# Optimization experiments

Hardware: AMD Instinct MI355X
Metric: run time of the kernel (lower is better)

The kernel has to match this reference:

```python
import jax, jax.numpy as jnp
import numpy as np

EMBED_DIM = 512
NUM_HEADS = 8
HEAD_DIM = EMBED_DIM // NUM_HEADS
SCALING = HEAD_DIM ** (-0.5)
LAMBDA = 1.0
T = 128
B = 8


def setup_inputs() -> dict:
    key = jax.random.key(0)
    ks = jax.random.split(key, 8)
    d = EMBED_DIM
    # xavier-uniform-ish scale for weights
    w_lim = float(np.sqrt(6.0 / (3 * d + d)))
    o_lim = float(np.sqrt(6.0 / (d + d)))
    return {
        "query": jax.random.normal(ks[0], (T, B, d), jnp.float32),
        "key": jax.random.normal(ks[1], (T, B, d), jnp.float32),
        "value": jax.random.normal(ks[2], (T, B, d), jnp.float32),
        "correlation_bias": jax.random.normal(ks[3], (B, T, T, T), jnp.float32) * 0.1,
        "in_proj_weight": jax.random.uniform(ks[4], (3 * d, d), jnp.float32, -w_lim, w_lim),
        "in_proj_bias": jnp.zeros((3 * d,), jnp.float32),
        "out_w": jax.random.uniform(ks[5], (d, d), jnp.float32, -o_lim, o_lim),
        "out_b": jnp.zeros((d,), jnp.float32),
    }


def reference(query, key, value, correlation_bias, in_proj_weight, in_proj_bias, out_w, out_b):
    tgt_len, bsz, d = query.shape
    h, hd = NUM_HEADS, HEAD_DIM
    # split packed in-projection
    q = query @ in_proj_weight[:d].T + in_proj_bias[:d]
    k = key @ in_proj_weight[d:2 * d].T + in_proj_bias[d:2 * d]
    v = value @ in_proj_weight[2 * d:].T + in_proj_bias[2 * d:]
    q = q * SCALING
    # [T, B, D] -> [B*H, T, hd]
    q = q.reshape(tgt_len, bsz * h, hd).transpose(1, 0, 2)
    k = k.reshape(tgt_len, bsz * h, hd).transpose(1, 0, 2)
    v = v.reshape(tgt_len, bsz * h, hd).transpose(1, 0, 2)
    # trilinear score cube: [B*H, Tq, Tk, Tv]
    scores = jnp.einsum('iat,ibt,ict->iabc', q, k, v)
    # expand correlation bias over heads: [B,Tq,Tk,Tv] -> [B*H,Tq,Tk,Tv]
    bias = jnp.broadcast_to(
        correlation_bias[:, None], (bsz, h, tgt_len, tgt_len, tgt_len)
    ).reshape(bsz * h, tgt_len, tgt_len, tgt_len)
    scores = scores + LAMBDA * bias
    # mean/max fusion over Tv, softmax over Tk
    fused = jnp.mean(scores, axis=-1) + jnp.max(scores, axis=-1)
    w = jax.nn.softmax(fused.astype(jnp.float32), axis=-1).astype(fused.dtype)
    # bmm with q (note: attends over q itself, Tk == Tq required)
    attn = jnp.einsum('iab,ibd->iad', w, q)
    attn = attn.transpose(1, 0, 2).reshape(tgt_len, bsz, d)
    return attn @ out_w.T + out_b
```

## Files before the change

### kernel.cpp

```cpp
#include <hip/hip_runtime.h>
#include <math.h>

#define SCALING 0.125f

typedef __attribute__((ext_vector_type(8))) short short8;
typedef __attribute__((ext_vector_type(4))) float f32x4;

static __device__ __forceinline__ unsigned short bf16r(float x) {
  unsigned int u = __float_as_uint(x);
  u += 0x7fffu + ((u >> 16) & 1u);
  return (unsigned short)(u >> 16);
}
static __device__ __forceinline__ float bf16f(unsigned short h) {
  return __uint_as_float(((unsigned int)h) << 16);
}
static __device__ __forceinline__ unsigned int pk_bf16(float lo, float hi) {
  unsigned int ua = __float_as_uint(lo);
  unsigned int ub = __float_as_uint(hi);
  ua += 0x7fffu + ((ua >> 16) & 1u);
  ub += 0x7fffu + ((ub >> 16) & 1u);
  return __builtin_amdgcn_perm(ub, ua, 0x07060302u);
}
static __device__ __forceinline__ void split4(float4 x, ushort4& h, ushort4& l) {
  h.x = bf16r(x.x); l.x = bf16r(x.x - bf16f(h.x));
  h.y = bf16r(x.y); l.y = bf16r(x.y - bf16f(h.y));
  h.z = bf16r(x.z); l.z = bf16r(x.z - bf16f(h.z));
  h.w = bf16r(x.w); l.w = bf16r(x.w - bf16f(h.w));
}
union U4S8 { uint4 u; short8 s; };

__global__ __launch_bounds__(256)
void prep_kernel(const float* __restrict__ query,
                 const float* __restrict__ key,
                 const float* __restrict__ value,
                 const float* __restrict__ W,
                 const float* __restrict__ out_w,
                 unsigned short* __restrict__ Xh,
                 unsigned short* __restrict__ Xl,
                 unsigned short* __restrict__ Wh,
                 unsigned short* __restrict__ Wl,
                 unsigned short* __restrict__ Owh,
                 unsigned short* __restrict__ Owl) {
  const int t = blockIdx.x * 256 + threadIdx.x;
  const int e = t * 4;
  const float* __restrict__ src;
  unsigned short *dh, *dl;
  if (e < 1572864) {
    const int g = e >> 19, j = e & 524287;
    src = (g == 0 ? query : g == 1 ? key : value) + j;
    dh = Xh + e; dl = Xl + e;
  } else if (e < 2359296) {
    const int j = e - 1572864;
    src = W + j; dh = Wh + j; dl = Wl + j;
  } else {
    const int j = e - 2359296;
    src = out_w + j; dh = Owh + j; dl = Owl + j;
  }
  const float4 v = *(const float4*)src;
  ushort4 hh, ll;
  split4(v, hh, ll);
  *(ushort4*)dh = hh;
  *(ushort4*)dl = ll;
}

__global__ __launch_bounds__(256)
void projmm_kernel(const unsigned short* __restrict__ Xh,
                   const unsigned short* __restrict__ Xl,
                   const unsigned short* __restrict__ Wh,
                   const unsigned short* __restrict__ Wl,
                   const float* __restrict__ bias,
                   float* __restrict__ qh, float* __restrict__ kh,
                   unsigned short* __restrict__ vh) {
  __shared__ __align__(16) unsigned short Ah[64 * 72];
  __shared__ __align__(16) unsigned short Al[64 * 72];
  __shared__ __align__(16) unsigned short Bh[32 * 72];
  __shared__ __align__(16) unsigned short Bl[32 * 72];
  const int n0 = blockIdx.x * 32;
  const int g = n0 >> 9;
  const unsigned short* __restrict__ Xgh = Xh + g * 524288;
  const unsigned short* __restrict__ Xgl = Xl + g * 524288;
  const int m0 = blockIdx.y * 64;
  const int tid = threadIdx.x;
  const int w = tid >> 6, lane = tid & 63;
  const int quad = lane >> 4, n15 = lane & 15;
  const int srow = tid >> 2;
  const int scol = (tid & 3) * 16;
  const bool doB = tid >= 128;
  const int brow = (tid & 127) >> 2;
  const int bcol = (tid & 3) * 16;

  f32x4 acc[2];
#pragma unroll
  for (int nt = 0; nt < 2; ++nt) acc[nt] = (f32x4){0.f, 0.f, 0.f, 0.f};

  uint4 rah0, rah1, ral0, ral1, rbh0, rbh1, rbl0, rbl1;
  {
    const int ar = (m0 + srow) * 512 + scol;
    rah0 = *(const uint4*)&Xgh[ar];   rah1 = *(const uint4*)&Xgh[ar + 8];
    ral0 = *(const uint4*)&Xgl[ar];   ral1 = *(const uint4*)&Xgl[ar + 8];
  }
  if (doB) {
    const int br = (n0 + brow) * 512 + bcol;
    rbh0 = *(const uint4*)&Wh[br];    rbh1 = *(const uint4*)&Wh[br + 8];
    rbl0 = *(const uint4*)&Wl[br];    rbl1 = *(const uint4*)&Wl[br + 8];
  }

  for (int k0 = 0; k0 < 512; k0 += 64) {
    __syncthreads();
    *(uint4*)&Ah[srow * 72 + scol] = rah0; *(uint4*)&Ah[srow * 72 + scol + 8] = rah1;
    *(uint4*)&Al[srow * 72 + scol] = ral0; *(uint4*)&Al[srow * 72 + scol + 8] = ral1;
    if (doB) {
      *(uint4*)&Bh[brow * 72 + bcol] = rbh0; *(uint4*)&Bh[brow * 72 + bcol + 8] = rbh1;
      *(uint4*)&Bl[brow * 72 + bcol] = rbl0; *(uint4*)&Bl[brow * 72 + bcol + 8] = rbl1;
    }
    __syncthreads();
    if (k0 + 64 < 512) {
      const int ar = (m0 + srow) * 512 + k0 + 64 + scol;
      rah0 = *(const uint4*)&Xgh[ar]; rah1 = *(const uint4*)&Xgh[ar + 8];
      ral0 = *(const uint4*)&Xgl[ar]; ral1 = *(const uint4*)&Xgl[ar + 8];
      if (doB) {
        const int br = (n0 + brow) * 512 + k0 + 64 + bcol;
        rbh0 = *(const uint4*)&Wh[br]; rbh1 = *(const uint4*)&Wh[br + 8];
        rbl0 = *(const uint4*)&Wl[br]; rbl1 = *(const uint4*)&Wl[br + 8];
      }
    }
#pragma unroll
    for (int kk = 0; kk < 2; ++kk) {
      short8 ah = *(const short8*)&Ah[(w * 16 + n15) * 72 + kk * 32 + quad * 8];
      short8 al = *(const short8*)&Al[(w * 16 + n15) * 72 + kk * 32 + quad * 8];
#pragma unroll
      for (int nt = 0; nt < 2; ++nt) {
        short8 bh = *(const short8*)&Bh[(nt * 16 + n15) * 72 + kk * 32 + quad * 8];
        short8 bl = *(const short8*)&Bl[(nt * 16 + n15) * 72 + kk * 32 + quad * 8];
        acc[nt] = __builtin_amdgcn_mfma_f32_16x16x32_bf16(ah, bh, acc[nt], 0, 0, 0);
        acc[nt] = __builtin_amdgcn_mfma_f32_16x16x32_bf16(ah, bl, acc[nt], 0, 0, 0);
        acc[nt] = __builtin_amdgcn_mfma_f32_16x16x32_bf16(al, bh, acc[nt], 0, 0, 0);
      }
    }
  }

#pragma unroll
  for (int nt = 0; nt < 2; ++nt) {
    const int j = n0 + nt * 16 + n15;
    const int jj = j & 511;
    const int head = jj >> 6;
    const int hd = jj & 63;
    const float bj = bias[j];
#pragma unroll
    for (int r = 0; r < 4; ++r) {
      const int row = m0 + w * 16 + quad * 4 + r;
      const int t = row >> 3;
      const int batch = row & 7;
      const int i = batch * 8 + head;
      const int idx = ((i << 7) + t) * 64 + hd;
      const float val = acc[nt][r] + bj;
      if (g == 0)      qh[idx] = val * SCALING;
      else if (g == 1) kh[idx] = val;
      else             vh[idx] = bf16r(val);
    }
  }
}

__global__ __launch_bounds__(256, 2)
void score_kernel(const float* __restrict__ qh,
                  const float* __restrict__ kh,
                  const unsigned short* __restrict__ vh,
                  const float* __restrict__ cbias,
                  unsigned short* __restrict__ attn_h,
                  unsigned short* __restrict__ attn_l) {
  __shared__ __align__(16) unsigned short Ks[2][128 * 72];
  __shared__ __align__(16) unsigned short Vs[2][128 * 72];
  __shared__ float rowS[8 * 128];

  const int ab = blockIdx.x;
  const int batch = ab >> 7;
  const int a = ab & 127;
  const int tid = threadIdx.x;
  const int w = tid >> 6;
  const int lane = tid & 63;
  const int quad = lane >> 4;
  const int n15 = lane & 15;
  const int col8 = (tid & 7) * 8;

  const float* __restrict__ bp = cbias + (size_t)ab * 16384;
  f32x4 biasReg[8][2];
#pragma unroll
  for (int ic = 0; ic < 8; ++ic)
#pragma unroll
    for (int jb = 0; jb < 2; ++jb) {
      const int b = w * 32 + jb * 16 + n15;
      biasReg[ic][jb] = *(const f32x4*)&bp[b * 128 + ic * 16 + quad * 4];
    }

  {
    const int i = batch * 8;
    const float* __restrict__ kb = kh + (size_t)i * 8192;
    const uint4* __restrict__ vb4 = (const uint4*)(vh + (size_t)i * 8192);
    const float* __restrict__ qa = qh + ((size_t)i * 128 + a) * 64;
    f32x4 q0 = *(const f32x4*)&qa[col8];
    f32x4 q1 = *(const f32x4*)&qa[col8 + 4];
#pragma unroll
    for (int j = 0; j < 4; ++j) {
      const int gg = j * 256 + tid;
      const int row = gg >> 3;
      *(uint4*)&Vs[0][row * 72 + col8] = vb4[gg];
      f32x4 k0 = *(const f32x4*)&kb[8 * gg];
      f32x4 k1 = *(const f32x4*)&kb[8 * gg + 4];
      k0 *= q0;
      k1 *= q1;
      uint4 pk;
      pk.x = pk_bf16(k0[0], k0[1]); pk.y = pk_bf16(k0[2], k0[3]);
      pk.z = pk_bf16(k1[0], k1[1]); pk.w = pk_bf16(k1[2], k1[3]);
      *(uint4*)&Ks[0][row * 72 + col8] = pk;
    }
  }
  __syncthreads();

  for (int h = 0; h < 8; ++h) {
    const int buf = h & 1;
    const int i = batch * 8 + h;

    uint4 vreg[4];
    f32x4 kreg[4][2];
    f32x4 qn0, qn1;
    if (h < 7) {
      const int in = i + 1;
      const float* __restrict__ kb = kh + (size_t)in * 8192;
      const uint4* __restrict__ vb4 = (const uint4*)(vh + (size_t)in * 8192);
      const float* __restrict__ qa = qh + ((size_t)in * 128 + a) * 64;
      qn0 = *(const f32x4*)&qa[col8];
      qn1 = *(const f32x4*)&qa[col8 + 4];
#pragma unroll
      for (int j = 0; j < 4; ++j) {
        const int gg = j * 256 + tid;
        vreg[j] = vb4[gg];
        kreg[j][0] = *(const f32x4*)&kb[8 * gg];
        kreg[j][1] = *(const f32x4*)&kb[8 * gg + 4];
      }
    }

    short8 bf[2][2];
#pragma unroll
    for (int jb = 0; jb < 2; ++jb)
#pragma unroll
      for (int kk = 0; kk < 2; ++kk)
        bf[jb][kk] = *(const short8*)&Ks[buf][(w * 32 + jb * 16 + n15) * 72 +
                                             kk * 32 + quad * 8];

    f32x4 acc[8][2];
#pragma unroll
    for (int ic = 0; ic < 8; ++ic) {
      short8 a0 = *(const short8*)&Vs[buf][(ic * 16 + n15) * 72 + quad * 8];
      short8 a1 = *(const short8*)&Vs[buf][(ic * 16 + n15) * 72 + 32 + quad * 8];
      acc[ic][0] = __builtin_amdgcn_mfma_f32_16x16x32_bf16(a0, bf[0][0], biasReg[ic][0], 0, 0, 0);
      acc[ic][0] = __builtin_amdgcn_mfma_f32_16x16x32_bf16(a1, bf[0][1], acc[ic][0], 0, 0, 0);
      acc[ic][1] = __builtin_amdgcn_mfma_f32_16x16x32_bf16(a0, bf[1][0], biasReg[ic][1], 0, 0, 0);
      acc[ic][1] = __builtin_amdgcn_mfma_f32_16x16x32_bf16(a1, bf[1][1], acc[ic][1], 0, 0, 0);
    }

    if (h < 7) {
      const int nb = buf ^ 1;
#pragma unroll
      for (int j = 0; j < 4; ++j) {
        const int gg = j * 256 + tid;
        const int row = gg >> 3;
        *(uint4*)&Vs[nb][row * 72 + col8] = vreg[j];
        kreg[j][0] *= qn0;
        kreg[j][1] *= qn1;
        uint4 pk;
        pk.x = pk_bf16(kreg[j][0][0], kreg[j][0][1]);
        pk.y = pk_bf16(kreg[j][0][2], kreg[j][0][3]);
        pk.z = pk_bf16(kreg[j][1][0], kreg[j][1][1]);
        pk.w = pk_bf16(kreg[j][1][2], kreg[j][1][3]);
        *(uint4*)&Ks[nb][row * 72 + col8] = pk;
      }
    }

    float fsum[2] = {0.f, 0.f};
    float fmx[2] = {-INFINITY, -INFINITY};
#pragma unroll
    for (int ic = 0; ic < 8; ++ic)
#pragma unroll
      for (int jb = 0; jb < 2; ++jb) {
        const float v0 = acc[ic][jb][0];
        const float v1 = acc[ic][jb][1];
        const float v2 = acc[ic][jb][2];
        const float v3 = acc[ic][jb][3];
        fsum[jb] += (v0 + v1) + (v2 + v3);
        fmx[jb] = fmaxf(fmx[jb], fmaxf(fmaxf(v0, v1), fmaxf(v2, v3)));
      }
#pragma unroll
    for (int off = 16; off <= 32; off <<= 1) {
#pragma unroll
      for (int jb = 0; jb < 2; ++jb) {
        fsum[jb] += __shfl_xor(fsum[jb], off, 64);
        fmx[jb] = fmaxf(fmx[jb], __shfl_xor(fmx[jb], off, 64));
      }
    }
    if (quad == 0) {
      rowS[h * 128 + w * 32 + n15] = fsum[0] * (1.0f / 128.0f) + fmx[0];
      rowS[h * 128 + w * 32 + 16 + n15] = fsum[1] * (1.0f / 128.0f) + fmx[1];
    }

    __syncthreads();
  }

#pragma unroll
  for (int hh = 0; hh < 2; ++hh) {
    const int h = w * 2 + hh;
    const int i = batch * 8 + h;
    float f0 = rowS[h * 128 + lane], f1 = rowS[h * 128 + 64 + lane];
    float m = fmaxf(f0, f1);
#pragma unroll
    for (int off = 32; off >= 1; off >>= 1) m = fmaxf(m, __shfl_xor(m, off, 64));
    const float e0 = expf(f0 - m), e1 = expf(f1 - m);
    float s = e0 + e1;
#pragma unroll
    for (int off = 32; off >= 1; off >>= 1) s += __shfl_xor(s, off, 64);
    const float inv = 1.0f / s;
    rowS[h * 128 + lane] = e0 * inv;
    rowS[h * 128 + 64 + lane] = e1 * inv;
    const float* __restrict__ qp = qh + (size_t)i * 8192 + lane;
    float acc2 = 0.0f;
#pragma unroll 8
    for (int b = 0; b < 128; ++b)
      acc2 = fmaf(rowS[h * 128 + b], qp[b * 64], acc2);
    const size_t idx = ((size_t)a * 8 + batch) * 512 + h * 64 + lane;
    const unsigned short hi = bf16r(acc2);
    attn_h[idx] = hi;
    attn_l[idx] = bf16r(acc2 - bf16f(hi));
  }
}

__global__ __launch_bounds__(256)
void outmm_kernel(const unsigned short* __restrict__ Xah,
                  const unsigned short* __restrict__ Xal,
                  const unsigned short* __restrict__ Owh,
                  const unsigned short* __restrict__ Owl,
                  const float* __restrict__ bias,
                  float* __restrict__ out) {
  __shared__ __align__(16) unsigned short Ah[64 * 72];
  __shared__ __align__(16) unsigned short Al[64 * 72];
  __shared__ __align__(16) unsigned short Bh[32 * 72];
  __shared__ __align__(16) unsigned short Bl[32 * 72];
  const int n0 = blockIdx.x * 32;
  const int m0 = blockIdx.y * 64;
  const int tid = threadIdx.x;
  const int w = tid >> 6, lane = tid & 63;
  const int quad = lane >> 4, n15 = lane & 15;
  const int srow = tid >> 2;
  const int scol = (tid & 3) * 16;
  const bool doB = tid >= 128;
  const int brow = (tid & 127) >> 2;
  const int bcol = (tid & 3) * 16;

  f32x4 acc[2];
#pragma unroll
  for (int nt = 0; nt < 2; ++nt) acc[nt] = (f32x4){0.f, 0.f, 0.f, 0.f};

  uint4 rah0, rah1, ral0, ral1, rbh0, rbh1, rbl0, rbl1;
  {
    const int ar = (m0 + srow) * 512 + scol;
    rah0 = *(const uint4*)&Xah[ar];   rah1 = *(const uint4*)&Xah[ar + 8];
    ral0 = *(const uint4*)&Xal[ar];   ral1 = *(const uint4*)&Xal[ar + 8];
  }
  if (doB) {
    const int br = (n0 + brow) * 512 + bcol;
    rbh0 = *(const uint4*)&Owh[br];   rbh1 = *(const uint4*)&Owh[br + 8];
    rbl0 = *(const uint4*)&Owl[br];   rbl1 = *(const uint4*)&Owl[br + 8];
  }

  for (int k0 = 0; k0 < 512; k0 += 64) {
    __syncthreads();
    *(uint4*)&Ah[srow * 72 + scol] = rah0; *(uint4*)&Ah[srow * 72 + scol + 8] = rah1;
    *(uint4*)&Al[srow * 72 + scol] = ral0; *(uint4*)&Al[srow * 72 + scol + 8] = ral1;
    if (doB) {
      *(uint4*)&Bh[brow * 72 + bcol] = rbh0; *(uint4*)&Bh[brow * 72 + bcol + 8] = rbh1;
      *(uint4*)&Bl[brow * 72 + bcol] = rbl0; *(uint4*)&Bl[brow * 72 + bcol + 8] = rbl1;
    }
    __syncthreads();
    if (k0 + 64 < 512) {
      const int ar = (m0 + srow) * 512 + k0 + 64 + scol;
      rah0 = *(const uint4*)&Xah[ar]; rah1 = *(const uint4*)&Xah[ar + 8];
      ral0 = *(const uint4*)&Xal[ar]; ral1 = *(const uint4*)&Xal[ar + 8];
      if (doB) {
        const int br = (n0 + brow) * 512 + k0 + 64 + bcol;
        rbh0 = *(const uint4*)&Owh[br]; rbh1 = *(const uint4*)&Owh[br + 8];
        rbl0 = *(const uint4*)&Owl[br]; rbl1 = *(const uint4*)&Owl[br + 8];
      }
    }
#pragma unroll
    for (int kk = 0; kk < 2; ++kk) {
      short8 ah = *(const short8*)&Ah[(w * 16 + n15) * 72 + kk * 32 + quad * 8];
      short8 al = *(const short8*)&Al[(w * 16 + n15) * 72 + kk * 32 + quad * 8];
#pragma unroll
      for (int nt = 0; nt < 2; ++nt) {
        short8 bh = *(const short8*)&Bh[(nt * 16 + n15) * 72 + kk * 32 + quad * 8];
        short8 bl = *(const short8*)&Bl[(nt * 16 + n15) * 72 + kk * 32 + quad * 8];
        acc[nt] = __builtin_amdgcn_mfma_f32_16x16x32_bf16(ah, bh, acc[nt], 0, 0, 0);
        acc[nt] = __builtin_amdgcn_mfma_f32_16x16x32_bf16(ah, bl, acc[nt], 0, 0, 0);
        acc[nt] = __builtin_amdgcn_mfma_f32_16x16x32_bf16(al, bh, acc[nt], 0, 0, 0);
      }
    }
  }

#pragma unroll
  for (int nt = 0; nt < 2; ++nt) {
    const int j = n0 + nt * 16 + n15;
    const float bj = bias[j];
#pragma unroll
    for (int r = 0; r < 4; ++r) {
      const int row = m0 + w * 16 + quad * 4 + r;
      out[(size_t)row * 512 + j] = acc[nt][r] + bj;
    }
  }
}

extern "C" void kernel_launch(void* const* d_in, const int* in_sizes, int n_in,
                              void* d_out, int out_size, void* d_ws,
                              size_t ws_size, hipStream_t stream) {
  const float* query = (const float*)d_in[0];
  const float* key   = (const float*)d_in[1];
  const float* value = (const float*)d_in[2];
  const float* cbias = (const float*)d_in[3];
  const float* W     = (const float*)d_in[4];
  const float* pb    = (const float*)d_in[5];
  const float* out_w = (const float*)d_in[6];
  const float* out_b = (const float*)d_in[7];
  float* out = (float*)d_out;

  float* ws = (float*)d_ws;
  float* qh = ws;
  float* kh = ws + 524288;
  unsigned short* vh     = (unsigned short*)(ws + 1048576);
  unsigned short* attn_h = (unsigned short*)(ws + 1310720);
  unsigned short* attn_l = (unsigned short*)(ws + 1572864);
  unsigned short* Xh     = (unsigned short*)(ws + 1835008);
  unsigned short* Xl     = (unsigned short*)(ws + 2621440);
  unsigned short* Wh     = (unsigned short*)(ws + 3407872);
  unsigned short* Wl     = (unsigned short*)(ws + 3801088);
  unsigned short* Owh    = (unsigned short*)(ws + 4194304);
  unsigned short* Owl    = (unsigned short*)(ws + 4325376);

  prep_kernel<<<2560, 256, 0, stream>>>(query, key, value, W, out_w,
                                        Xh, Xl, Wh, Wl, Owh, Owl);
  projmm_kernel<<<dim3(48, 16), 256, 0, stream>>>(Xh, Xl, Wh, Wl, pb,
                                                  qh, kh, vh);
  score_kernel<<<1024, 256, 0, stream>>>(qh, kh, vh, cbias, attn_h, attn_l);
  outmm_kernel<<<dim3(16, 16), 256, 0, stream>>>(attn_h, attn_l, Owh, Owl,
                                                 out_b, out);
}
```

Baseline: 181.1 us.

## Use async global-to-LDS loads with double-buffered swizzled tiles in projection GEMMs

The projection and output GEMM kernels now stage tiles through global_load_lds direct-to-LDS copies into two shared-memory buffers, replacing the register round-trip staging. The next k-tile is prefetched while MFMAs run on the current one, and there is now one barrier per iteration instead of two. An XOR swizzle on 16-byte column groups replaces the padded row stride to avoid LDS bank conflicts. The cost is twice the shared memory per block, which may lower occupancy, and the code now relies on the async LDS load builtin and its ordering with the barrier.

```diff
diff --git a/kernel.cpp b/kernel.cpp
--- a/kernel.cpp
+++ b/kernel.cpp
@@ -28,6 +28,13 @@
   h.w = bf16r(x.w); l.w = bf16r(x.w - bf16f(h.w));
 }
 union U4S8 { uint4 u; short8 s; };
+
+static __device__ __forceinline__ void gload16(const unsigned short* g,
+                                               unsigned short* l) {
+  __builtin_amdgcn_global_load_lds(
+      (const __attribute__((address_space(1))) void*)(g),
+      (__attribute__((address_space(3))) void*)(l), 16, 0, 0);
+}
 
 __global__ __launch_bounds__(256)
 void prep_kernel(const float* __restrict__ query,
@@ -71,10 +78,7 @@
                    const float* __restrict__ bias,
                    float* __restrict__ qh, float* __restrict__ kh,
                    unsigned short* __restrict__ vh) {
-  __shared__ __align__(16) unsigned short Ah[64 * 72];
-  __shared__ __align__(16) unsigned short Al[64 * 72];
-  __shared__ __align__(16) unsigned short Bh[32 * 72];
-  __shared__ __align__(16) unsigned short Bl[32 * 72];
+  __shared__ __align__(16) unsigned short S[2][12288];
   const int n0 = blockIdx.x * 32;
   const int g = n0 >> 9;
   const unsigned short* __restrict__ Xgh = Xh + g * 524288;
@@ -83,59 +87,59 @@
   const int tid = threadIdx.x;
   const int w = tid >> 6, lane = tid & 63;
   const int quad = lane >> 4, n15 = lane & 15;
-  const int srow = tid >> 2;
-  const int scol = (tid & 3) * 16;
-  const bool doB = tid >= 128;
-  const int brow = (tid & 127) >> 2;
-  const int bcol = (tid & 3) * 16;
+  const int lrow = lane >> 3;
+  const int colOff = ((lane & 7) ^ lrow) * 8;
+
+  const unsigned short* gb[6];
+  int lo[6];
+#pragma unroll
+  for (int j = 0; j < 6; ++j) {
+    const int c = w * 6 + j;
+    const unsigned short* gsrc;
+    int off, grow;
+    if (c < 8)       { gsrc = Xgh; off = c * 512;              grow = m0 + c * 8; }
+    else if (c < 16) { gsrc = Xgl; off = 4096 + (c - 8) * 512;  grow = m0 + (c - 8) * 8; }
+    else if (c < 20) { gsrc = Wh;  off = 8192 + (c - 16) * 512; grow = n0 + (c - 16) * 8; }
+    else             { gsrc = Wl;  off = 10240 + (c - 20) * 512; grow = n0 + (c - 20) * 8; }
+    gb[j] = gsrc + (size_t)(grow + lrow) * 512 + colOff;
+    lo[j] = off;
+  }
 
   f32x4 acc[2];
 #pragma unroll
   for (int nt = 0; nt < 2; ++nt) acc[nt] = (f32x4){0.f, 0.f, 0.f, 0.f};
 
-  uint4 rah0, rah1, ral0, ral1, rbh0, rbh1, rbl0, rbl1;
-  {
-    const int ar = (m0 + srow) * 512 + scol;
-    rah0 = *(const uint4*)&Xgh[ar];   rah1 = *(const uint4*)&Xgh[ar + 8];
-    ral0 = *(const uint4*)&Xgl[ar];   ral1 = *(const uint4*)&Xgl[ar + 8];
-  }
-  if (doB) {
-    const int br = (n0 + brow) * 512 + bcol;
-    rbh0 = *(const uint4*)&Wh[br];    rbh1 = *(const uint4*)&Wh[br + 8];
-    rbl0 = *(const uint4*)&Wl[br];    rbl1 = *(const uint4*)&Wl[br + 8];
-  }
-
+#pragma unroll
+  for (int j = 0; j < 6; ++j) gload16(gb[j], &S[0][lo[j]]);
+  __syncthreads();
+
+  const int rA = w * 16 + n15;
+  const int swz = n15 & 7;
+  int side = 0;
   for (int k0 = 0; k0 < 512; k0 += 64) {
-    __syncthreads();
-    *(uint4*)&Ah[srow * 72 + scol] = rah0; *(uint4*)&Ah[srow * 72 + scol + 8] = rah1;
-    *(uint4*)&Al[srow * 72 + scol] = ral0; *(uint4*)&Al[srow * 72 + scol + 8] = ral1;
-    if (doB) {
-      *(uint4*)&Bh[brow * 72 + bcol] = rbh0; *(uint4*)&Bh[brow * 72 + bcol + 8] = rbh1;
-      *(uint4*)&Bl[brow * 72 + bcol] = rbl0; *(uint4*)&Bl[brow * 72 + bcol + 8] = rbl1;
-    }
-    __syncthreads();
     if (k0 + 64 < 512) {
-      const int ar = (m0 + srow) * 512 + k0 + 64 + scol;
-      rah0 = *(const uint4*)&Xgh[ar]; rah1 = *(const uint4*)&Xgh[ar + 8];
-      ral0 = *(const uint4*)&Xgl[ar]; ral1 = *(const uint4*)&Xgl[ar + 8];
-      if (doB) {
-        const int br = (n0 + brow) * 512 + k0 + 64 + bcol;
-        rbh0 = *(const uint4*)&Wh[br]; rbh1 = *(const uint4*)&Wh[br + 8];
-        rbl0 = *(const uint4*)&Wl[br]; rbl1 = *(const uint4*)&Wl[br + 8];
-      }
+      const int ns = side ^ 1;
+#pragma unroll
+      for (int j = 0; j < 6; ++j) gload16(gb[j] + k0 + 64, &S[ns][lo[j]]);
     }
 #pragma unroll
     for (int kk = 0; kk < 2; ++kk) {
-      short8 ah = *(const short8*)&Ah[(w * 16 + n15) * 72 + kk * 32 + quad * 8];
-      short8 al = *(const short8*)&Al[(w * 16 + n15) * 72 + kk * 32 + quad * 8];
+      const int gA0 = ((kk * 4 + quad) ^ swz) * 8;
+      short8 ah = *(const short8*)&S[side][rA * 64 + gA0];
+      short8 al = *(const short8*)&S[side][4096 + rA * 64 + gA0];
 #pragma unroll
       for (int nt = 0; nt < 2; ++nt) {
-        short8 bh = *(const short8*)&Bh[(nt * 16 + n15) * 72 + kk * 32 + quad * 8];
-        short8 bl = *(const short8*)&Bl[(nt * 16 + n15) * 72 + kk * 32 + quad * 8];
+        const int rB = nt * 16 + n15;
+        short8 bh = *(const short8*)&S[side][8192 + rB * 64 + gA0];
+        short8 bl = *(const short8*)&S[side][10240 + rB * 64 + gA0];
         acc[nt] = __builtin_amdgcn_mfma_f32_16x16x32_bf16(ah, bh, acc[nt], 0, 0, 0);
         acc[nt] = __builtin_amdgcn_mfma_f32_16x16x32_bf16(ah, bl, acc[nt], 0, 0, 0);
         acc[nt] = __builtin_amdgcn_mfma_f32_16x16x32_bf16(al, bh, acc[nt], 0, 0, 0);
       }
+    }
+    if (k0 + 64 < 512) {
+      __syncthreads();
+      side ^= 1;
     }
   }
 
@@ -339,68 +343,65 @@
                   const unsigned short* __restrict__ Owl,
                   const float* __restrict__ bias,
                   float* __restrict__ out) {
-  __shared__ __align__(16) unsigned short Ah[64 * 72];
-  __shared__ __align__(16) unsigned short Al[64 * 72];
-  __shared__ __align__(16) unsigned short Bh[32 * 72];
-  __shared__ __align__(16) unsigned short Bl[32 * 72];
+  __shared__ __align__(16) unsigned short S[2][12288];
   const int n0 = blockIdx.x * 32;
   const int m0 = blockIdx.y * 64;
   const int tid = threadIdx.x;
   const int w = tid >> 6, lane = tid & 63;
   const int quad = lane >> 4, n15 = lane & 15;
-  const int srow = tid >> 2;
-  const int scol = (tid & 3) * 16;
-  const bool doB = tid >= 128;
-  const int brow = (tid & 127) >> 2;
-  const int bcol = (tid & 3) * 16;
+  const int lrow = lane >> 3;
+  const int colOff = ((lane & 7) ^ lrow) * 8;
+
+  const unsigned short* gb[6];
+  int lo[6];
+#pragma unroll
+  for (int j = 0; j < 6; ++j) {
+    const int c = w * 6 + j;
+    const unsigned short* gsrc;
+    int off, grow;
+    if (c < 8)       { gsrc = Xah; off = c * 512;               grow = m0 + c * 8; }
+    else if (c < 16) { gsrc = Xal; off = 4096 + (c - 8) * 512;   grow = m0 + (c - 8) * 8; }
+    else if (c < 20) { gsrc = Owh; off = 8192 + (c - 16) * 512;  grow = n0 + (c - 16) * 8; }
+    else             { gsrc = Owl; off = 10240 + (c - 20) * 512; grow = n0 + (c - 20) * 8; }
+    gb[j] = gsrc + (size_t)(grow + lrow) * 512 + colOff;
+    lo[j] = off;
+  }
 
   f32x4 acc[2];
 #pragma unroll
   for (int nt = 0; nt < 2; ++nt) acc[nt] = (f32x4){0.f, 0.f, 0.f, 0.f};
 
-  uint4 rah0, rah1, ral0, ral1, rbh0, rbh1, rbl0, rbl1;
-  {
-    const int ar = (m0 + srow) * 512 + scol;
-    rah0 = *(const uint4*)&Xah[ar];   rah1 = *(const uint4*)&Xah[ar + 8];
-    ral0 = *(const uint4*)&Xal[ar];   ral1 = *(const uint4*)&Xal[ar + 8];
-  }
-  if (doB) {
-    const int br = (n0 + brow) * 512 + bcol;
-    rbh0 = *(const uint4*)&Owh[br];   rbh1 = *(const uint4*)&Owh[br + 8];
-    rbl0 = *(const uint4*)&Owl[br];   rbl1 = *(const uint4*)&Owl[br + 8];
-  }
-
+#pragma unroll
+  for (int j = 0; j < 6; ++j) gload16(gb[j], &S[0][lo[j]]);
+  __syncthreads();
+
+  const int rA = w * 16 + n15;
+  const int swz = n15 & 7;
+  int side = 0;
   for (int k0 = 0; k0 < 512; k0 += 64) {
-    __syncthreads();
-    *(uint4*)&Ah[srow * 72 + scol] = rah0; *(uint4*)&Ah[srow * 72 + scol + 8] = rah1;
-    *(uint4*)&Al[srow * 72 + scol] = ral0; *(uint4*)&Al[srow * 72 + scol + 8] = ral1;
-    if (doB) {
-      *(uint4*)&Bh[brow * 72 + bcol] = rbh0; *(uint4*)&Bh[brow * 72 + bcol + 8] = rbh1;
-      *(uint4*)&Bl[brow * 72 + bcol] = rbl0; *(uint4*)&Bl[brow * 72 + bcol + 8] = rbl1;
-    }
-    __syncthreads();
     if (k0 + 64 < 512) {
-      const int ar = (m0 + srow) * 512 + k0 + 64 + scol;
-      rah0 = *(const uint4*)&Xah[ar]; rah1 = *(const uint4*)&Xah[ar + 8];
-      ral0 = *(const uint4*)&Xal[ar]; ral1 = *(const uint4*)&Xal[ar + 8];
-      if (doB) {
-        const int br = (n0 + brow) * 512 + k0 + 64 + bcol;
-        rbh0 = *(const uint4*)&Owh[br]; rbh1 = *(const uint4*)&Owh[br + 8];
-        rbl0 = *(const uint4*)&Owl[br]; rbl1 = *(const uint4*)&Owl[br + 8];
-      }
+      const int ns = side ^ 1;
+#pragma unroll
+      for (int j = 0; j < 6; ++j) gload16(gb[j] + k0 + 64, &S[ns][lo[j]]);
     }
 #pragma unroll
     for (int kk = 0; kk < 2; ++kk) {
-      short8 ah = *(const short8*)&Ah[(w * 16 + n15) * 72 + kk * 32 + quad * 8];
-      short8 al = *(const short8*)&Al[(w * 16 + n15) * 72 + kk * 32 + quad * 8];
+      const int gA0 = ((kk * 4 + quad) ^ swz) * 8;
+      short8 ah = *(const short8*)&S[side][rA * 64 + gA0];
+      short8 al = *(const short8*)&S[side][4096 + rA * 64 + gA0];
 #pragma unroll
       for (int nt = 0; nt < 2; ++nt) {
-        short8 bh = *(const short8*)&Bh[(nt * 16 + n15) * 72 + kk * 32 + quad * 8];
-        short8 bl = *(const short8*)&Bl[(nt * 16 + n15) * 72 + kk * 32 + quad * 8];
+        const int rB = nt * 16 + n15;
+        short8 bh = *(const short8*)&S[side][8192 + rB * 64 + gA0];
+        short8 bl = *(const short8*)&S[side][10240 + rB * 64 + gA0];
         acc[nt] = __builtin_amdgcn_mfma_f32_16x16x32_bf16(ah, bh, acc[nt], 0, 0, 0);
         acc[nt] = __builtin_amdgcn_mfma_f32_16x16x32_bf16(ah, bl, acc[nt], 0, 0, 0);
         acc[nt] = __builtin_amdgcn_mfma_f32_16x16x32_bf16(al, bh, acc[nt], 0, 0, 0);
       }
+    }
+    if (k0 + 64 < 512) {
+      __syncthreads();
+      side ^= 1;
     }
   }
 
```

Result: no change. 178.8 us (-1.3%).
